# Kernel tuning notes

Hardware: AMD Instinct MI355X
Metric: run time of the kernel (lower is better)

Reference implementation:

```python
import jax, jax.numpy as jnp
import numpy as np

B, N, H, HEADS = 4, 2048, 1024, 16
D = H // HEADS  # head dim = 64

def rotate_half(x):
    x1, x2 = jnp.split(x, 2, axis=-1)
    return jnp.concatenate((-x2, x1), axis=-1)

def apply_rope(pos, t):
    # pos: [n, d] broadcasts against t: [b, h, n, d]
    return t * jnp.cos(pos) + rotate_half(t) * jnp.sin(pos)

def setup_inputs() -> dict:
    key = jax.random.key(0)
    k1, k2, k3, k4 = jax.random.split(key, 4)
    x = jax.random.normal(k1, (B, N, H), dtype=jnp.float32)
    rotary_emb = jax.random.normal(k2, (N, D), dtype=jnp.float32)
    # torch Linear(H, 3H, bias=False): weight [3H, H], y = x @ W.T
    w_qkv = jax.random.normal(k3, (3 * H, H), dtype=jnp.float32) * (1.0 / np.sqrt(H))
    w_out = jax.random.normal(k4, (H, H), dtype=jnp.float32) * (1.0 / np.sqrt(H))
    return {"x": x, "rotary_emb": rotary_emb, "w_qkv": w_qkv, "w_out": w_out}

def reference(x, rotary_emb, w_qkv, w_out):
    qkv = jnp.einsum('bnh,oh->bno', x, w_qkv)  # [B, N, 3H]
    q, k, v = jnp.split(qkv, 3, axis=-1)
    def split_heads(t):
        return t.reshape(B, N, HEADS, D).transpose(0, 2, 1, 3)  # b h n d
    q, k, v = map(split_heads, (q, k, v))
    q = apply_rope(rotary_emb, q)
    k = apply_rope(rotary_emb, k)
    scale = 1.0 / np.sqrt(D).astype(np.float32)
    scores = jnp.einsum('bhqd,bhkd->bhqk', q, k) * scale
    attn = jax.nn.softmax(scores, axis=-1)
    out = jnp.einsum('bhqk,bhkd->bhqd', attn, v)
    out = out.transpose(0, 2, 1, 3).reshape(B, N, H)  # b n (h d)
    return jnp.einsum('bnh,oh->bno', out, w_out)
```

## Files before the change

### kernel.cpp

```cpp
#include <hip/hip_runtime.h>
#include <hip/hip_fp16.h>
#include <stdint.h>

#define DEVI __device__ __forceinline__

using f16x2 = __attribute__((ext_vector_type(2))) _Float16;
using f16x8 = __attribute__((ext_vector_type(8))) _Float16;
using f32x4 = __attribute__((ext_vector_type(4))) float;
using f32x16 = __attribute__((ext_vector_type(16))) float;
using u32x4 = __attribute__((ext_vector_type(4))) uint32_t;

DEVI void gload_lds16(const void* g, void* lds) {
  using GP = const __attribute__((address_space(1))) void*;
  using LP = __attribute__((address_space(3))) void*;
  __builtin_amdgcn_global_load_lds((GP)g, (LP)lds, 16, 0, 0);
}

DEVI uint32_t pack2h(float a, float b) {
  return (uint32_t)__half_as_ushort(__float2half(a)) |
         ((uint32_t)__half_as_ushort(__float2half(b)) << 16);
}

DEVI uint32_t cvtpk(float a, float b) {
  auto h2 = __builtin_amdgcn_cvt_pkrtz(a, b);
  return __builtin_bit_cast(uint32_t, h2);
}

DEVI void plswap(uint32_t& a, uint32_t& b) {
  asm volatile("v_permlane32_swap_b32 %0, %1" : "+v"(a), "+v"(b));
}

DEVI float dot2acc(uint32_t w, f16x2 one, float c) {
  return __builtin_amdgcn_fdot2(__builtin_bit_cast(f16x2, w), one, c, false);
}

DEVI float fmax3(float a, float b, float c) { return fmaxf(fmaxf(a, b), c); }

__global__ __launch_bounds__(256) void cvt_f32_f16(const float* __restrict__ in,
                                                   __half* __restrict__ out, int n8) {
  int i = blockIdx.x * 256 + threadIdx.x;
  if (i >= n8) return;
  float4 a = ((const float4*)in)[i * 2];
  float4 b = ((const float4*)in)[i * 2 + 1];
  uint4 u;
  u.x = pack2h(a.x, a.y);
  u.y = pack2h(a.z, a.w);
  u.z = pack2h(b.x, b.y);
  u.w = pack2h(b.z, b.w);
  ((uint4*)out)[i] = u;
}

#define GEMM_CORE(A_, B_, K_)                                                           \
  __shared__ __half As[128 * 64];                                                       \
  __shared__ __half Bs[128 * 64];                                                       \
  const int tid = threadIdx.x;                                                          \
  const int w = tid >> 6, l = tid & 63;                                                 \
  const int wm = w >> 1, wn = w & 1;                                                    \
  const int m16 = l & 15, g = l >> 4;                                                   \
  const int row0 = blockIdx.y * 128, col0 = blockIdx.x * 128;                           \
  const int srow = l >> 3;                                                              \
  const int ks = ((l & 7) ^ srow) * 8;                                                  \
  f32x4 acc[4][4] = {};                                                                 \
  for (int kt = 0; kt < (K_); kt += 64) {                                               \
    __syncthreads();                                                                    \
    _Pragma("unroll") for (int i = 0; i < 4; ++i) {                                     \
      int c = w * 4 + i;                                                                \
      int r = c * 8 + srow;                                                             \
      gload_lds16((A_) + (size_t)(row0 + r) * (K_) + kt + ks, (char*)As + c * 1024);    \
      gload_lds16((B_) + (size_t)(col0 + r) * (K_) + kt + ks, (char*)Bs + c * 1024);    \
    }                                                                                   \
    __syncthreads();                                                                    \
    _Pragma("unroll") for (int kk = 0; kk < 2; ++kk) {                                  \
      f16x8 aF[4], bF[4];                                                               \
      _Pragma("unroll") for (int mi = 0; mi < 4; ++mi) {                                \
        int r = wm * 64 + mi * 16 + m16;                                                \
        aF[mi] = *(const f16x8*)((const char*)As + r * 128 + (((kk * 4 + g) ^ (r & 7)) << 4)); \
      }                                                                                 \
      _Pragma("unroll") for (int ni = 0; ni < 4; ++ni) {                                \
        int r = wn * 64 + ni * 16 + m16;                                                \
        bF[ni] = *(const f16x8*)((const char*)Bs + r * 128 + (((kk * 4 + g) ^ (r & 7)) << 4)); \
      }                                                                                 \
      _Pragma("unroll") for (int mi = 0; mi < 4; ++mi)                                  \
          _Pragma("unroll") for (int ni = 0; ni < 4; ++ni)                              \
              acc[mi][ni] = __builtin_amdgcn_mfma_f32_16x16x32_f16(aF[mi], bF[ni],      \
                                                                   acc[mi][ni], 0, 0, 0); \
    }                                                                                   \
  }

__global__ __launch_bounds__(256) void gemm_qkv_rope(const __half* __restrict__ A,
                                                     const __half* __restrict__ B,
                                                     const float* __restrict__ rot,
                                                     __half* __restrict__ qr,
                                                     __half* __restrict__ kr,
                                                     __half* __restrict__ vr) {
  GEMM_CORE(A, B, 1024)

  const int s = blockIdx.x >> 3;
  const int hh = (blockIdx.x & 7) * 2 + wn;
  if (s < 2) {
    const float sc = (s == 0) ? 0.18033688011112042f : 1.0f;
    __half* base = (s == 0) ? qr : kr;
#pragma unroll
    for (int mi = 0; mi < 4; ++mi)
#pragma unroll
      for (int j = 0; j < 4; ++j) {
        int r = row0 + wm * 64 + mi * 16 + g * 4 + j;
        int n = r & 2047;
        int bh = (r >> 11) * 16 + hh;
        __half* orow = base + ((size_t)bh * 2048 + n) * 64;
        const float* rp = rot + n * 64;
#pragma unroll
        for (int ni = 0; ni < 2; ++ni) {
          int dlo = ni * 16 + m16;
          float xlo = acc[mi][ni][j], xhi = acc[mi][ni + 2][j];
          float s0, c0, s1, c1;
          __sincosf(rp[dlo], &s0, &c0);
          __sincosf(rp[dlo + 32], &s1, &c1);
          orow[dlo]      = __float2half((xlo * c0 - xhi * s0) * sc);
          orow[dlo + 32] = __float2half((xhi * c1 + xlo * s1) * sc);
        }
      }
  } else {
#pragma unroll
    for (int mi = 0; mi < 4; ++mi)
#pragma unroll
      for (int j = 0; j < 4; ++j) {
        int r = row0 + wm * 64 + mi * 16 + g * 4 + j;
        int n = r & 2047;
        int bh = (r >> 11) * 16 + hh;
        __half* vcol = vr + ((size_t)bh * 64) * 2048 + n;
#pragma unroll
        for (int ni = 0; ni < 4; ++ni) {
          int d = ni * 16 + m16;
          vcol[(size_t)d * 2048] = __float2half(acc[mi][ni][j]);
        }
      }
  }
}

__global__ __launch_bounds__(256) void gemm_bt_f32(const __half* __restrict__ A,
                                                   const __half* __restrict__ B,
                                                   float* __restrict__ C, int N, int K) {
  GEMM_CORE(A, B, K)
#pragma unroll
  for (int mi = 0; mi < 4; ++mi)
#pragma unroll
    for (int ni = 0; ni < 4; ++ni)
#pragma unroll
      for (int j = 0; j < 4; ++j) {
        int r = row0 + wm * 64 + mi * 16 + g * 4 + j;
        int cc = col0 + wn * 64 + ni * 16 + m16;
        C[(size_t)r * N + cc] = acc[mi][ni][j];
      }
}

__global__ __launch_bounds__(256, 4) void attn_fwd(const __half* __restrict__ qr,
                                                   const __half* __restrict__ kr,
                                                   const __half* __restrict__ vr,
                                                   __half* __restrict__ out) {
  __shared__ __half K2[2 * 64 * 64];
  __shared__ __half V2[2 * 64 * 64];

  int bid = blockIdx.x;
  bid = (bid & 7) * 128 + (bid >> 3);
  const int bh = bid >> 4;
  const int q0 = (bid & 15) * 128;
  const int tid = threadIdx.x;
  const int w = tid >> 6, l = tid & 63;
  const int q = l & 31, hi = l >> 5;
  const size_t headoff = (size_t)bh * 2048 * 64;

  f16x8 qB[4];
  {
    const __half* qp = qr + headoff + (size_t)(q0 + w * 32 + q) * 64 + hi * 8;
#pragma unroll
    for (int c = 0; c < 4; ++c) qB[c] = *(const f16x8*)(qp + c * 16);
  }

  int kf[4];
#pragma unroll
  for (int c = 0; c < 4; ++c)
    kf[c] = q * 128 + 16 * (hi ^ (q & 1)) + 32 * (c ^ ((q >> 1) & 3));
  const int vbase = q * 128 + ((hi ^ (q & 7)) << 4);

  const int krow_l = l >> 3, kslot = l & 7;
  const __half* kb = kr + headoff;
  const __half* vb = vr + (size_t)bh * 64 * 2048;

  auto STAGE = [&](int buf, int kv0) {
#pragma unroll
    for (int i = 0; i < 2; ++i) {
      int c = w * 2 + i;
      int row = c * 8 + krow_l;
      gload_lds16(kb + (size_t)(kv0 + row) * 64 + ((kslot ^ (row & 7)) * 8),
                  (char*)K2 + buf * 8192 + c * 1024);
    }
#pragma unroll
    for (int i = 0; i < 2; ++i) {
      int c = w * 2 + i;
      int d = c * 8 + (l >> 3);
      gload_lds16(vb + (size_t)d * 2048 + kv0 + (((l & 7) ^ (l >> 3)) * 8),
                  (char*)V2 + buf * 8192 + c * 1024);
    }
  };

  const f16x2 one2 = {(_Float16)1.f, (_Float16)1.f};
  f32x16 o0 = {}, o1 = {};
  float mreg = -1e30f, lreg = 0.f;

  STAGE(0, 0);
  __syncthreads();

  for (int t = 0; t < 32; ++t) {
    const int buf = t & 1;
    if (t < 31) STAGE(buf ^ 1, (t + 1) * 64);

    const char* Kb = (const char*)K2 + buf * 8192;
    const char* Vb = (const char*)V2 + buf * 8192;
#pragma unroll
    for (int kvb = 0; kvb < 2; ++kvb) {
      f32x16 s = {};
      __builtin_amdgcn_s_setprio(1);
#pragma unroll
      for (int c = 0; c < 4; ++c) {
        f16x8 kA = *(const f16x8*)(Kb + kvb * 4096 + kf[c]);
        s = __builtin_amdgcn_mfma_f32_32x32x16_f16(kA, qB[c], s, 0, 0, 0);
      }
      __builtin_amdgcn_s_setprio(0);

      float mt = fmax3(s[0], s[1], s[2]);
      mt = fmax3(mt, s[3], s[4]);
      mt = fmax3(mt, s[5], s[6]);
      mt = fmax3(mt, s[7], s[8]);
      mt = fmax3(mt, s[9], s[10]);
      mt = fmax3(mt, s[11], s[12]);
      mt = fmax3(mt, s[13], s[14]);
      mt = fmaxf(mt, s[15]);
      mt = fmaxf(mt, __shfl_xor(mt, 32));
      if (__any(mt - mreg > 8.f)) {
        float mnew = fmaxf(mreg, mt);
        float alpha = __builtin_amdgcn_exp2f(mreg - mnew);
        lreg *= alpha;
        o0 *= alpha;
        o1 *= alpha;
        mreg = mnew;
      }
      uint32_t W[8];
      float rs = 0.f;
#pragma unroll
      for (int i2 = 0; i2 < 8; ++i2) {
        float e0 = __builtin_amdgcn_exp2f(s[2 * i2] - mreg);
        float e1 = __builtin_amdgcn_exp2f(s[2 * i2 + 1] - mreg);
        W[i2] = cvtpk(e0, e1);
        rs = dot2acc(W[i2], one2, rs);
      }
      rs += __shfl_xor(rs, 32);
      lreg += rs;

      plswap(W[0], W[2]);
      plswap(W[1], W[3]);
      plswap(W[4], W[6]);
      plswap(W[5], W[7]);
      u32x4 f0 = {W[0], W[1], W[2], W[3]};
      u32x4 f1 = {W[4], W[5], W[6], W[7]};
      f16x8 pA0 = __builtin_bit_cast(f16x8, f0);
      f16x8 pA1 = __builtin_bit_cast(f16x8, f1);

      const int vx = vbase ^ (kvb << 6);
      const int vx2 = vx ^ 32;
      f16x8 v00 = *(const f16x8*)(Vb + vx);
      f16x8 v01 = *(const f16x8*)(Vb + vx + 4096);
      f16x8 v10 = *(const f16x8*)(Vb + vx2);
      f16x8 v11 = *(const f16x8*)(Vb + vx2 + 4096);
      __builtin_amdgcn_s_setprio(1);
      o0 = __builtin_amdgcn_mfma_f32_32x32x16_f16(pA0, v00, o0, 0, 0, 0);
      o1 = __builtin_amdgcn_mfma_f32_32x32x16_f16(pA0, v01, o1, 0, 0, 0);
      o0 = __builtin_amdgcn_mfma_f32_32x32x16_f16(pA1, v10, o0, 0, 0, 0);
      o1 = __builtin_amdgcn_mfma_f32_32x32x16_f16(pA1, v11, o1, 0, 0, 0);
      __builtin_amdgcn_s_setprio(0);
    }

    __syncthreads();
  }

  const int b = bh >> 4, hh = bh & 15;
  float invl = 1.0f / lreg;
#pragma unroll
  for (int r = 0; r < 16; ++r) {
    int qrow = (r & 3) + 8 * (r >> 2) + 4 * hi;
    float inv = __shfl(invl, qrow);
    __half* orow = out + (size_t)(b * 2048 + q0 + w * 32 + qrow) * 1024 + hh * 64;
    orow[q] = __float2half(o0[r] * inv);
    orow[32 + q] = __float2half(o1[r] * inv);
  }
}

extern "C" void kernel_launch(void* const* d_in, const int* in_sizes, int n_in,
                              void* d_out, int out_size, void* d_ws, size_t ws_size,
                              hipStream_t stream) {
  const float* x    = (const float*)d_in[0];
  const float* rot  = (const float*)d_in[1];
  const float* wqkv = (const float*)d_in[2];
  const float* wout = (const float*)d_in[3];
  float* out = (float*)d_out;
  char* ws = (char*)d_ws;

  __half* xb    = (__half*)(ws + 0);
  __half* wqkvb = (__half*)(ws + (16ull << 20));
  __half* woutb = (__half*)(ws + (22ull << 20));
  __half* qr    = (__half*)(ws + (24ull << 20));
  __half* ao    = (__half*)(ws + (40ull << 20));
  __half* kr    = (__half*)(ws + (72ull << 20));
  __half* vr    = (__half*)(ws + (88ull << 20));

  cvt_f32_f16<<<4096, 256, 0, stream>>>(x, xb, 1048576);
  cvt_f32_f16<<<1536, 256, 0, stream>>>(wqkv, wqkvb, 393216);
  cvt_f32_f16<<<512, 256, 0, stream>>>(wout, woutb, 131072);
  gemm_qkv_rope<<<dim3(24, 64), 256, 0, stream>>>(xb, wqkvb, rot, qr, kr, vr);
  attn_fwd<<<1024, 256, 0, stream>>>(qr, kr, vr, ao);
  gemm_bt_f32<<<dim3(8, 64), 256, 0, stream>>>(ao, woutb, out, 1024, 1024);
}
```

Before: 217.6 us.

## Use 128x64 tiles for output GEMM and permlane swaps for softmax reductions

Replaces the output projection GEMM (M=8192, N=1024) with a 128x64-tile kernel, so 1024 blocks launch instead of 512 and the 256 CUs are better filled. Each wave computes a 32x64 slice with 16x16x32 MFMAs and XOR-swizzled LDS loads. In attention, the cross-half max and sum reductions switch from __shfl_xor (which goes through LDS permute) to a v_mov plus v_permlane32_swap. The smaller tiles cut per-block data reuse and raise total global traffic for the GEMM.

```diff
diff --git a/kernel.cpp b/kernel.cpp
--- a/kernel.cpp
+++ b/kernel.cpp
@@ -28,6 +28,19 @@
 
 DEVI void plswap(uint32_t& a, uint32_t& b) {
   asm volatile("v_permlane32_swap_b32 %0, %1" : "+v"(a), "+v"(b));
+}
+
+DEVI float xhalf_max(float t) {
+  float u;
+  asm volatile("v_mov_b32 %0, %1" : "=v"(u) : "v"(t));
+  asm volatile("v_permlane32_swap_b32 %0, %1" : "+v"(t), "+v"(u));
+  return fmaxf(t, u);
+}
+DEVI float xhalf_sum(float t) {
+  float u;
+  asm volatile("v_mov_b32 %0, %1" : "=v"(u) : "v"(t));
+  asm volatile("v_permlane32_swap_b32 %0, %1" : "+v"(t), "+v"(u));
+  return t + u;
 }
 
 DEVI float dot2acc(uint32_t w, f16x2 one, float c) {
@@ -138,18 +151,64 @@
   }
 }
 
-__global__ __launch_bounds__(256) void gemm_bt_f32(const __half* __restrict__ A,
-                                                   const __half* __restrict__ B,
-                                                   float* __restrict__ C, int N, int K) {
-  GEMM_CORE(A, B, K)
-#pragma unroll
-  for (int mi = 0; mi < 4; ++mi)
+__global__ __launch_bounds__(256) void gemm_bt64_f32(const __half* __restrict__ A,
+                                                     const __half* __restrict__ B,
+                                                     float* __restrict__ C, int N, int K) {
+  __shared__ __half As[128 * 64];
+  __shared__ __half Bs[64 * 64];
+  const int tid = threadIdx.x;
+  const int w = tid >> 6, l = tid & 63;
+  const int m16 = l & 15, g = l >> 4;
+  const int row0 = blockIdx.y * 128, col0 = blockIdx.x * 64;
+  const int srow = l >> 3;
+  const int ks = ((l & 7) ^ srow) * 8;
+
+  f32x4 acc[2][4] = {};
+
+  for (int kt = 0; kt < K; kt += 64) {
+    __syncthreads();
+#pragma unroll
+    for (int i = 0; i < 4; ++i) {
+      int c = w * 4 + i;
+      int r = c * 8 + srow;
+      gload_lds16(A + (size_t)(row0 + r) * K + kt + ks, (char*)As + c * 1024);
+    }
+#pragma unroll
+    for (int i = 0; i < 2; ++i) {
+      int c = w * 2 + i;
+      int r = c * 8 + srow;
+      gload_lds16(B + (size_t)(col0 + r) * K + kt + ks, (char*)Bs + c * 1024);
+    }
+    __syncthreads();
+#pragma unroll
+    for (int kk = 0; kk < 2; ++kk) {
+      f16x8 aF[2], bF[4];
+#pragma unroll
+      for (int mi = 0; mi < 2; ++mi) {
+        int r = w * 32 + mi * 16 + m16;
+        aF[mi] = *(const f16x8*)((const char*)As + r * 128 + (((kk * 4 + g) ^ (r & 7)) << 4));
+      }
+#pragma unroll
+      for (int ni = 0; ni < 4; ++ni) {
+        int r = ni * 16 + m16;
+        bF[ni] = *(const f16x8*)((const char*)Bs + r * 128 + (((kk * 4 + g) ^ (r & 7)) << 4));
+      }
+#pragma unroll
+      for (int mi = 0; mi < 2; ++mi)
+#pragma unroll
+        for (int ni = 0; ni < 4; ++ni)
+          acc[mi][ni] = __builtin_amdgcn_mfma_f32_16x16x32_f16(aF[mi], bF[ni], acc[mi][ni], 0, 0, 0);
+    }
+  }
+
+#pragma unroll
+  for (int mi = 0; mi < 2; ++mi)
 #pragma unroll
     for (int ni = 0; ni < 4; ++ni)
 #pragma unroll
       for (int j = 0; j < 4; ++j) {
-        int r = row0 + wm * 64 + mi * 16 + g * 4 + j;
-        int cc = col0 + wn * 64 + ni * 16 + m16;
+        int r = row0 + w * 32 + mi * 16 + g * 4 + j;
+        int cc = col0 + ni * 16 + m16;
         C[(size_t)r * N + cc] = acc[mi][ni][j];
       }
 }
@@ -236,7 +295,7 @@
       mt = fmax3(mt, s[11], s[12]);
       mt = fmax3(mt, s[13], s[14]);
       mt = fmaxf(mt, s[15]);
-      mt = fmaxf(mt, __shfl_xor(mt, 32));
+      mt = xhalf_max(mt);
       if (__any(mt - mreg > 8.f)) {
         float mnew = fmaxf(mreg, mt);
         float alpha = __builtin_amdgcn_exp2f(mreg - mnew);
@@ -254,8 +313,7 @@
         W[i2] = cvtpk(e0, e1);
         rs = dot2acc(W[i2], one2, rs);
       }
-      rs += __shfl_xor(rs, 32);
-      lreg += rs;
+      lreg += xhalf_sum(rs);
 
       plswap(W[0], W[2]);
       plswap(W[1], W[3]);
@@ -318,5 +376,5 @@
   cvt_f32_f16<<<512, 256, 0, stream>>>(wout, woutb, 131072);
   gemm_qkv_rope<<<dim3(24, 64), 256, 0, stream>>>(xb, wqkvb, rot, qr, kr, vr);
   attn_fwd<<<1024, 256, 0, stream>>>(qr, kr, vr, ao);
-  gemm_bt_f32<<<dim3(8, 64), 256, 0, stream>>>(ao, woutb, out, 1024, 1024);
-}
+  gemm_bt64_f32<<<dim3(16, 64), 256, 0, stream>>>(ao, woutb, out, 1024, 1024);
+}
```

New measurement: 228.6 us. 5.1% more time.
